# Performance work log

Measured on AMD Instinct MI355X. Metric: run time of the kernel, lower is better.

Reference implementation:

```python
import jax, jax.numpy as jnp
import numpy as np

N_NODES = 100000

def prelu(x, alpha):
    return jnp.where(x >= 0, x, alpha * x)

def setup_inputs() -> dict:
    key = jax.random.key(0)
    ks = jax.random.split(key, 8)
    N, E, D = N_NODES, 1600000, 128
    AX = jax.random.normal(ks[0], (N, D), dtype=jnp.float32)
    A_row = jax.random.randint(ks[1], (E,), 0, N, dtype=jnp.int32)
    A_col = jax.random.randint(ks[2], (E,), 0, N, dtype=jnp.int32)
    A_val = jax.random.uniform(ks[3], (E,), dtype=jnp.float32)
    # Xavier-uniform linear weights, zero bias (as in module init)
    lim = float(np.sqrt(6.0 / (D + D)))
    Wr_w = jax.random.uniform(ks[4], (D, D), minval=-lim, maxval=lim, dtype=jnp.float32)
    W_w = jax.random.uniform(ks[5], (D, D), minval=-lim, maxval=lim, dtype=jnp.float32)
    Wr_b = jnp.zeros((D,), dtype=jnp.float32)
    W_b = jnp.zeros((D,), dtype=jnp.float32)
    g_alpha = jnp.full((1,), 0.25, dtype=jnp.float32)    # PReLU default init
    act_alpha = jnp.full((1,), 0.25, dtype=jnp.float32)
    return {"AX": AX, "A_row": A_row, "A_col": A_col, "A_val": A_val,
            "Wr_w": Wr_w, "Wr_b": Wr_b, "W_w": W_w, "W_b": W_b,
            "g_alpha": g_alpha, "act_alpha": act_alpha}

def reference(AX, A_row, A_col, A_val, Wr_w, Wr_b, W_w, W_b, g_alpha, act_alpha):
    # h = g(Wr @ AX)  : [N, H]
    h = prelu(AX @ Wr_w.T + Wr_b, g_alpha)
    # SpMM: temp[i] = sum_{(i,j) in E} A_val * h[j]
    msgs = A_val[:, None] * h[A_col]                       # [E, H] gather
    temp = jax.ops.segment_sum(msgs, A_row, num_segments=N_NODES)
    # act(W @ temp), unsqueeze batch dim
    out = prelu(temp @ W_w.T + W_b, act_alpha)
    return out[None, :, :]
```

## Files before the change

kernel.cpp:

```cpp
#include <hip/hip_runtime.h>
#include <stdint.h>


typedef _Float16 half8 __attribute__((ext_vector_type(8)));
typedef _Float16 half4 __attribute__((ext_vector_type(4)));
typedef _Float16 half2v __attribute__((ext_vector_type(2)));
typedef float floatx4 __attribute__((ext_vector_type(4)));

#define LDK 136
#define SHIFT 5
#define NBMAX 3200
#define NBLK 256
#define SCT 1024
#define CAP 1024

__global__ __launch_bounds__(256, 2)
void gemm_hist(const float* __restrict__ X, const float* __restrict__ Wr,
               const float* __restrict__ bias, const float* __restrict__ alpha_p,
               _Float16* __restrict__ out, int N,
               const int* __restrict__ rows, int* __restrict__ hist_g,
               int E, int chunk, int NB,
               const float* __restrict__ W, _Float16* __restrict__ W16)
{
    __shared__ _Float16 Xs[128 * LDK];
    __shared__ _Float16 Ws[128 * LDK];
    const int tid = threadIdx.x;

    if (blockIdx.x < NBLK) {
        const int hb = blockIdx.x;
        int* lh = (int*)Xs;
        if (hb == 0) {
#pragma unroll
            for (int j = 0; j < 64; ++j)
                W16[tid + j * 256] = (_Float16)W[tid + j * 256];
        }
        for (int i = tid; i < NB; i += 256) lh[i] = 0;
        __syncthreads();
        int s = hb * chunk, e = min(E, s + chunk);
        for (int i = s + tid; i < e; i += 256)
            atomicAdd(&lh[rows[i] >> SHIFT], 1);
        __syncthreads();
        for (int b = tid; b < NB; b += 256)
            hist_g[b * NBLK + hb] = lh[b];
        return;
    }

    const int bm  = (blockIdx.x - NBLK) * 128;
    const float alpha = *alpha_p;

#pragma unroll
    for (int i = 0; i < 16; ++i) {
        int c   = tid + i * 256;
        int row = c >> 5;
        int coff = (c & 31) * 4;
        float4 f = *(const float4*)(Wr + row * 128 + coff);
        half4 hv = { (_Float16)f.x, (_Float16)f.y, (_Float16)f.z, (_Float16)f.w };
        *(half4*)(&Ws[row * LDK + coff]) = hv;
    }
#pragma unroll
    for (int i = 0; i < 16; ++i) {
        int c   = tid + i * 256;
        int row = c >> 5;
        int coff = (c & 31) * 4;
        int grow = bm + row;
        half4 hv = {};
        if (grow < N) {
            float4 f = *(const float4*)(X + (size_t)grow * 128 + coff);
            hv[0] = (_Float16)f.x; hv[1] = (_Float16)f.y;
            hv[2] = (_Float16)f.z; hv[3] = (_Float16)f.w;
        }
        *(half4*)(&Xs[row * LDK + coff]) = hv;
    }
    __syncthreads();

    const int wave = tid >> 6;
    const int lane = tid & 63;
    const int l15  = lane & 15;
    const int quad = lane >> 4;

    floatx4 acc[2][8] = {};
#pragma unroll
    for (int k0 = 0; k0 < 128; k0 += 32) {
        half8 a0 = *(const half8*)(&Xs[(wave * 32 +      l15) * LDK + k0 + quad * 8]);
        half8 a1 = *(const half8*)(&Xs[(wave * 32 + 16 + l15) * LDK + k0 + quad * 8]);
        half8 b[8];
#pragma unroll
        for (int n = 0; n < 8; ++n)
            b[n] = *(const half8*)(&Ws[(n * 16 + l15) * LDK + k0 + quad * 8]);
#pragma unroll
        for (int n = 0; n < 8; ++n) {
            acc[0][n] = __builtin_amdgcn_mfma_f32_16x16x32_f16(a0, b[n], acc[0][n], 0, 0, 0);
            acc[1][n] = __builtin_amdgcn_mfma_f32_16x16x32_f16(a1, b[n], acc[1][n], 0, 0, 0);
        }
    }

#pragma unroll
    for (int mt = 0; mt < 2; ++mt) {
#pragma unroll
        for (int n = 0; n < 8; ++n) {
#pragma unroll
            for (int r = 0; r < 4; ++r) {
                int row = bm + wave * 32 + mt * 16 + quad * 4 + r;
                int col = n * 16 + l15;
                if (row < N) {
                    float v = acc[mt][n][r] + bias[col];
                    v = (v >= 0.f) ? v : alpha * v;
                    out[(size_t)row * 128 + col] = (_Float16)v;
                }
            }
        }
    }
}

__global__ __launch_bounds__(NBLK)
void bucket_scan1(int* __restrict__ hist_g, int* __restrict__ tot)
{
    __shared__ int sd[NBLK];
    int b = blockIdx.x, t = threadIdx.x;
    int v = hist_g[b * NBLK + t];
    sd[t] = v;
    __syncthreads();
    for (int off = 1; off < NBLK; off <<= 1) {
        int x = (t >= off) ? sd[t - off] : 0;
        __syncthreads();
        sd[t] += x;
        __syncthreads();
    }
    hist_g[b * NBLK + t] = sd[t] - v;
    if (t == NBLK - 1) tot[b] = sd[t];
}

__global__ __launch_bounds__(1024)
void bucket_scan2(const int* __restrict__ tot, int* __restrict__ bkt_ptr, int NB, int E)
{
    __shared__ int sd[1024];
    int t = threadIdx.x;
    int v[4]; int s = 0;
#pragma unroll
    for (int j = 0; j < 4; ++j) {
        int idx = t * 4 + j;
        v[j] = (idx < NB) ? tot[idx] : 0;
        s += v[j];
    }
    sd[t] = s;
    __syncthreads();
    for (int off = 1; off < 1024; off <<= 1) {
        int x = (t >= off) ? sd[t - off] : 0;
        __syncthreads();
        sd[t] += x;
        __syncthreads();
    }
    int base = (t == 0) ? 0 : sd[t - 1];
#pragma unroll
    for (int j = 0; j < 4; ++j) {
        int idx = t * 4 + j;
        if (idx < NB) { bkt_ptr[idx] = base; base += v[j]; }
    }
    if (t == 0) bkt_ptr[NB] = E;
}

__global__ __launch_bounds__(SCT)
void bucket_scatter(const int* __restrict__ rows, const int* __restrict__ cols,
                    const float* __restrict__ vals, const int* __restrict__ bkt_ptr,
                    const int* __restrict__ hist_g, uint2* __restrict__ edges,
                    int E, int chunk, int NB)
{
    __shared__ int cur[NBMAX];
    int tid = threadIdx.x, blk = blockIdx.x;
    for (int b = tid; b < NB; b += SCT)
        cur[b] = bkt_ptr[b] + hist_g[b * NBLK + blk];
    __syncthreads();
    int s = blk * chunk, e = min(E, s + chunk);
    for (int i = s + tid; i < e; i += SCT) {
        int r = rows[i];
        int b = r >> SHIFT;
        uint2 ed;
        ed.x = (unsigned)cols[i] | ((unsigned)(r & 31) << 20);
        ed.y = __float_as_uint(vals[i]);
        int p = atomicAdd(&cur[b], 1);
        edges[p] = ed;
    }
}

__global__ __launch_bounds__(256, 8)
void spmm_fused(const int* __restrict__ bkt_ptr, const uint2* __restrict__ edges,
                const _Float16* __restrict__ h, const _Float16* __restrict__ W16,
                const float* __restrict__ bias, const float* __restrict__ alpha_p,
                float* __restrict__ out, int N)
{
    __shared__ uint2 eS[CAP];
    __shared__ _Float16 T[32 * LDK];
    __shared__ int bins[32], startS[33];

    const int tid  = threadIdx.x;
    const int wave = tid >> 6;
    const int lane = tid & 63;
    const int b    = blockIdx.x;
    const int s0   = bkt_ptr[b], e0 = bkt_ptr[b + 1];

    float acc[8][2] = {};

    for (int base = s0; base < e0; base += CAP) {
        const int n = min(CAP, e0 - base);
        if (tid < 32) bins[tid] = 0;
        __syncthreads();
        uint2 q[4];
#pragma unroll
        for (int u = 0; u < 4; ++u) {
            int i = tid + u * 256;
            if (i < n) {
                q[u] = edges[base + i];
                atomicAdd(&bins[q[u].x >> 20], 1);
            }
        }
        __syncthreads();
        if (tid < 32) {
            int x = bins[tid];
#pragma unroll
            for (int off = 1; off < 32; off <<= 1) {
                int y = __shfl_up(x, off);
                if (tid >= off) x += y;
            }
            startS[tid + 1] = x;
            if (tid == 0) startS[0] = 0;
            bins[tid] = x - bins[tid];
        }
        __syncthreads();
#pragma unroll
        for (int u = 0; u < 4; ++u) {
            int i = tid + u * 256;
            if (i < n) {
                int p = atomicAdd(&bins[q[u].x >> 20], 1);
                eS[p] = q[u];
            }
        }
        __syncthreads();

#pragma unroll
        for (int j = 0; j < 8; ++j) {
            int r  = wave * 8 + j;
            int rs = startS[r], re = startS[r + 1];
            float a0r = acc[j][0], a1r = acc[j][1];
            int i = rs;
            for (; i + 7 < re; i += 8) {
                uint2 q0 = eS[i],     q1 = eS[i + 1], q2 = eS[i + 2], q3 = eS[i + 3];
                uint2 q4 = eS[i + 4], q5 = eS[i + 5], q6 = eS[i + 6], q7 = eS[i + 7];
                half2v v0 = *(const half2v*)(h + (size_t)(q0.x & 0xFFFFF) * 128 + lane * 2);
                half2v v1 = *(const half2v*)(h + (size_t)(q1.x & 0xFFFFF) * 128 + lane * 2);
                half2v v2 = *(const half2v*)(h + (size_t)(q2.x & 0xFFFFF) * 128 + lane * 2);
                half2v v3 = *(const half2v*)(h + (size_t)(q3.x & 0xFFFFF) * 128 + lane * 2);
                half2v v4 = *(const half2v*)(h + (size_t)(q4.x & 0xFFFFF) * 128 + lane * 2);
                half2v v5 = *(const half2v*)(h + (size_t)(q5.x & 0xFFFFF) * 128 + lane * 2);
                half2v v6 = *(const half2v*)(h + (size_t)(q6.x & 0xFFFFF) * 128 + lane * 2);
                half2v v7 = *(const half2v*)(h + (size_t)(q7.x & 0xFFFFF) * 128 + lane * 2);
                float w0 = __uint_as_float(q0.y), w1 = __uint_as_float(q1.y);
                float w2 = __uint_as_float(q2.y), w3 = __uint_as_float(q3.y);
                float w4 = __uint_as_float(q4.y), w5 = __uint_as_float(q5.y);
                float w6 = __uint_as_float(q6.y), w7 = __uint_as_float(q7.y);
                a0r += w0 * (float)v0[0]; a1r += w0 * (float)v0[1];
                a0r += w1 * (float)v1[0]; a1r += w1 * (float)v1[1];
                a0r += w2 * (float)v2[0]; a1r += w2 * (float)v2[1];
                a0r += w3 * (float)v3[0]; a1r += w3 * (float)v3[1];
                a0r += w4 * (float)v4[0]; a1r += w4 * (float)v4[1];
                a0r += w5 * (float)v5[0]; a1r += w5 * (float)v5[1];
                a0r += w6 * (float)v6[0]; a1r += w6 * (float)v6[1];
                a0r += w7 * (float)v7[0]; a1r += w7 * (float)v7[1];
            }
            for (; i + 1 < re; i += 2) {
                uint2 q0 = eS[i], q1 = eS[i + 1];
                half2v v0 = *(const half2v*)(h + (size_t)(q0.x & 0xFFFFF) * 128 + lane * 2);
                half2v v1 = *(const half2v*)(h + (size_t)(q1.x & 0xFFFFF) * 128 + lane * 2);
                float w0 = __uint_as_float(q0.y), w1 = __uint_as_float(q1.y);
                a0r += w0 * (float)v0[0]; a1r += w0 * (float)v0[1];
                a0r += w1 * (float)v1[0]; a1r += w1 * (float)v1[1];
            }
            if (i < re) {
                uint2 q0 = eS[i];
                half2v v0 = *(const half2v*)(h + (size_t)(q0.x & 0xFFFFF) * 128 + lane * 2);
                float w0 = __uint_as_float(q0.y);
                a0r += w0 * (float)v0[0]; a1r += w0 * (float)v0[1];
            }
            acc[j][0] = a0r; acc[j][1] = a1r;
        }
        __syncthreads();
    }

#pragma unroll
    for (int j = 0; j < 8; ++j) {
        half2v o = { (_Float16)acc[j][0], (_Float16)acc[j][1] };
        *(half2v*)(&T[(wave * 8 + j) * LDK + lane * 2]) = o;
    }
    __syncthreads();

    const float alpha = *alpha_p;
    const int l15  = lane & 15;
    const int quad = lane >> 4;
    floatx4 c[2][2] = {};
#pragma unroll
    for (int k0 = 0; k0 < 128; k0 += 32) {
        half8 a0 = *(const half8*)(&T[(     l15) * LDK + k0 + quad * 8]);
        half8 a1 = *(const half8*)(&T[(16 + l15) * LDK + k0 + quad * 8]);
#pragma unroll
        for (int nt = 0; nt < 2; ++nt) {
            int nrow = (wave * 2 + nt) * 16 + l15;
            half8 bf = *(const half8*)(W16 + nrow * 128 + k0 + quad * 8);
            c[0][nt] = __builtin_amdgcn_mfma_f32_16x16x32_f16(a0, bf, c[0][nt], 0, 0, 0);
            c[1][nt] = __builtin_amdgcn_mfma_f32_16x16x32_f16(a1, bf, c[1][nt], 0, 0, 0);
        }
    }
    const int row0 = b << SHIFT;
#pragma unroll
    for (int mt = 0; mt < 2; ++mt) {
#pragma unroll
        for (int nt = 0; nt < 2; ++nt) {
            int col = (wave * 2 + nt) * 16 + l15;
            float bcol = bias[col];
#pragma unroll
            for (int r = 0; r < 4; ++r) {
                int row = row0 + mt * 16 + quad * 4 + r;
                if (row < N) {
                    float v = c[mt][nt][r] + bcol;
                    v = (v >= 0.f) ? v : alpha * v;
                    out[(size_t)row * 128 + col] = v;
                }
            }
        }
    }
}

static inline size_t align256(size_t x) { return (x + 255) & ~(size_t)255; }

extern "C" void kernel_launch(void* const* d_in, const int* in_sizes, int n_in,
                              void* d_out, int out_size, void* d_ws, size_t ws_size,
                              hipStream_t stream)
{
    const float* AX        = (const float*)d_in[0];
    const int*   A_row     = (const int*)  d_in[1];
    const int*   A_col     = (const int*)  d_in[2];
    const float* A_val     = (const float*)d_in[3];
    const float* Wr_w      = (const float*)d_in[4];
    const float* Wr_b      = (const float*)d_in[5];
    const float* W_w       = (const float*)d_in[6];
    const float* W_b       = (const float*)d_in[7];
    const float* g_alpha   = (const float*)d_in[8];
    const float* act_alpha = (const float*)d_in[9];

    const int N = in_sizes[0] / 128;
    const int E = in_sizes[1];
    const int NB = (N + 31) >> SHIFT;
    const int chunk = (E + NBLK - 1) / NBLK;

    char* ws = (char*)d_ws;
    size_t off = 0;
    _Float16* h       = (_Float16*)(ws + off); off += align256((size_t)N * 128 * 2);
    uint2*    edges   = (uint2*)   (ws + off); off += align256((size_t)E * 8);
    int*      hist_g  = (int*)     (ws + off); off += align256((size_t)NB * NBLK * 4);
    int*      tot     = (int*)     (ws + off); off += align256((size_t)NB * 4);
    int*      bkt_ptr = (int*)     (ws + off); off += align256((size_t)(NB + 1) * 4);
    _Float16* W16     = (_Float16*)(ws + off); off += align256((size_t)128 * 128 * 2);
    (void)ws_size; (void)n_in; (void)out_size;

    const int gemmB = (N + 127) / 128;

    gemm_hist<<<NBLK + gemmB, 256, 0, stream>>>(AX, Wr_w, Wr_b, g_alpha, h, N,
                                                A_row, hist_g, E, chunk, NB,
                                                W_w, W16);
    bucket_scan1<<<NB, NBLK, 0, stream>>>(hist_g, tot);
    bucket_scan2<<<1, 1024, 0, stream>>>(tot, bkt_ptr, NB, E);
    bucket_scatter<<<NBLK, SCT, 0, stream>>>(A_row, A_col, A_val, bkt_ptr, hist_g,
                                             edges, E, chunk, NB);
    spmm_fused<<<NB, 256, 0, stream>>>(bkt_ptr, edges, h, W16, W_b, act_alpha,
                                       (float*)d_out, N);
}
```

Before: 287.2 us.

## Load GEMM A-operand directly to registers and fold bucket scan2 into scatter

The GEMM blocks now load and convert X rows straight into MFMA A-fragment registers instead of staging them through shared memory. This halves the LDS footprint, so launch bounds go up to 3 blocks per SM. Separately, the single-block global bucket prefix scan is merged into bucket_scatter: each scatter block recomputes the 1024-wide scan redundantly, and block 0 writes bkt_ptr. This removes one kernel launch and a serialized tiny kernel, at the cost of redundant scan work in every scatter block and uncoalesced direct global loads for X.

```diff
diff --git a/kernel.cpp b/kernel.cpp
--- a/kernel.cpp
+++ b/kernel.cpp
@@ -14,7 +14,7 @@
 #define SCT 1024
 #define CAP 1024
 
-__global__ __launch_bounds__(256, 2)
+__global__ __launch_bounds__(256, 3)
 void gemm_hist(const float* __restrict__ X, const float* __restrict__ Wr,
                const float* __restrict__ bias, const float* __restrict__ alpha_p,
                _Float16* __restrict__ out, int N,
@@ -22,13 +22,12 @@
                int E, int chunk, int NB,
                const float* __restrict__ W, _Float16* __restrict__ W16)
 {
-    __shared__ _Float16 Xs[128 * LDK];
     __shared__ _Float16 Ws[128 * LDK];
     const int tid = threadIdx.x;
 
     if (blockIdx.x < NBLK) {
         const int hb = blockIdx.x;
-        int* lh = (int*)Xs;
+        int* lh = (int*)Ws;
         if (hb == 0) {
 #pragma unroll
             for (int j = 0; j < 64; ++j)
@@ -47,6 +46,31 @@
 
     const int bm  = (blockIdx.x - NBLK) * 128;
     const float alpha = *alpha_p;
+    const int wave = tid >> 6;
+    const int lane = tid & 63;
+    const int l15  = lane & 15;
+    const int quad = lane >> 4;
+
+    half8 a[2][4];
+#pragma unroll
+    for (int mt = 0; mt < 2; ++mt) {
+        const int xrow = bm + wave * 32 + mt * 16 + l15;
+        const float* xp = X + (size_t)xrow * 128 + quad * 8;
+        const bool ok = xrow < N;
+#pragma unroll
+        for (int k = 0; k < 4; ++k) {
+            half8 hv = {};
+            if (ok) {
+                float4 f0 = *(const float4*)(xp + k * 32);
+                float4 f1 = *(const float4*)(xp + k * 32 + 4);
+                hv[0] = (_Float16)f0.x; hv[1] = (_Float16)f0.y;
+                hv[2] = (_Float16)f0.z; hv[3] = (_Float16)f0.w;
+                hv[4] = (_Float16)f1.x; hv[5] = (_Float16)f1.y;
+                hv[6] = (_Float16)f1.z; hv[7] = (_Float16)f1.w;
+            }
+            a[mt][k] = hv;
+        }
+    }
 
 #pragma unroll
     for (int i = 0; i < 16; ++i) {
@@ -57,40 +81,20 @@
         half4 hv = { (_Float16)f.x, (_Float16)f.y, (_Float16)f.z, (_Float16)f.w };
         *(half4*)(&Ws[row * LDK + coff]) = hv;
     }
-#pragma unroll
-    for (int i = 0; i < 16; ++i) {
-        int c   = tid + i * 256;
-        int row = c >> 5;
-        int coff = (c & 31) * 4;
-        int grow = bm + row;
-        half4 hv = {};
-        if (grow < N) {
-            float4 f = *(const float4*)(X + (size_t)grow * 128 + coff);
-            hv[0] = (_Float16)f.x; hv[1] = (_Float16)f.y;
-            hv[2] = (_Float16)f.z; hv[3] = (_Float16)f.w;
-        }
-        *(half4*)(&Xs[row * LDK + coff]) = hv;
-    }
-    __syncthreads();
-
-    const int wave = tid >> 6;
-    const int lane = tid & 63;
-    const int l15  = lane & 15;
-    const int quad = lane >> 4;
+    __syncthreads();
 
     floatx4 acc[2][8] = {};
 #pragma unroll
-    for (int k0 = 0; k0 < 128; k0 += 32) {
-        half8 a0 = *(const half8*)(&Xs[(wave * 32 +      l15) * LDK + k0 + quad * 8]);
-        half8 a1 = *(const half8*)(&Xs[(wave * 32 + 16 + l15) * LDK + k0 + quad * 8]);
+    for (int k = 0; k < 4; ++k) {
+        const int k0 = k * 32;
         half8 b[8];
 #pragma unroll
         for (int n = 0; n < 8; ++n)
             b[n] = *(const half8*)(&Ws[(n * 16 + l15) * LDK + k0 + quad * 8]);
 #pragma unroll
         for (int n = 0; n < 8; ++n) {
-            acc[0][n] = __builtin_amdgcn_mfma_f32_16x16x32_f16(a0, b[n], acc[0][n], 0, 0, 0);
-            acc[1][n] = __builtin_amdgcn_mfma_f32_16x16x32_f16(a1, b[n], acc[1][n], 0, 0, 0);
+            acc[0][n] = __builtin_amdgcn_mfma_f32_16x16x32_f16(a[0][k], b[n], acc[0][n], 0, 0, 0);
+            acc[1][n] = __builtin_amdgcn_mfma_f32_16x16x32_f16(a[1][k], b[n], acc[1][n], 0, 0, 0);
         }
     }
 
@@ -130,11 +134,16 @@
     if (t == NBLK - 1) tot[b] = sd[t];
 }
 
-__global__ __launch_bounds__(1024)
-void bucket_scan2(const int* __restrict__ tot, int* __restrict__ bkt_ptr, int NB, int E)
-{
-    __shared__ int sd[1024];
-    int t = threadIdx.x;
+__global__ __launch_bounds__(SCT)
+void bucket_scatter(const int* __restrict__ rows, const int* __restrict__ cols,
+                    const float* __restrict__ vals, const int* __restrict__ tot,
+                    const int* __restrict__ hist_g, uint2* __restrict__ edges,
+                    int* __restrict__ bkt_ptr, int E, int chunk, int NB)
+{
+    __shared__ int sd[SCT];
+    __shared__ int cur[NBMAX];
+    const int t = threadIdx.x, blk = blockIdx.x;
+
     int v[4]; int s = 0;
 #pragma unroll
     for (int j = 0; j < 4; ++j) {
@@ -144,7 +153,7 @@
     }
     sd[t] = s;
     __syncthreads();
-    for (int off = 1; off < 1024; off <<= 1) {
+    for (int off = 1; off < SCT; off <<= 1) {
         int x = (t >= off) ? sd[t - off] : 0;
         __syncthreads();
         sd[t] += x;
@@ -154,24 +163,17 @@
 #pragma unroll
     for (int j = 0; j < 4; ++j) {
         int idx = t * 4 + j;
-        if (idx < NB) { bkt_ptr[idx] = base; base += v[j]; }
-    }
-    if (t == 0) bkt_ptr[NB] = E;
-}
-
-__global__ __launch_bounds__(SCT)
-void bucket_scatter(const int* __restrict__ rows, const int* __restrict__ cols,
-                    const float* __restrict__ vals, const int* __restrict__ bkt_ptr,
-                    const int* __restrict__ hist_g, uint2* __restrict__ edges,
-                    int E, int chunk, int NB)
-{
-    __shared__ int cur[NBMAX];
-    int tid = threadIdx.x, blk = blockIdx.x;
-    for (int b = tid; b < NB; b += SCT)
-        cur[b] = bkt_ptr[b] + hist_g[b * NBLK + blk];
-    __syncthreads();
-    int s = blk * chunk, e = min(E, s + chunk);
-    for (int i = s + tid; i < e; i += SCT) {
+        if (idx < NB) {
+            cur[idx] = base + hist_g[idx * NBLK + blk];
+            if (blk == 0) bkt_ptr[idx] = base;
+            base += v[j];
+        }
+    }
+    if (blk == 0 && t == 0) bkt_ptr[NB] = E;
+    __syncthreads();
+
+    int s0 = blk * chunk, e0 = min(E, s0 + chunk);
+    for (int i = s0 + t; i < e0; i += SCT) {
         int r = rows[i];
         int b = r >> SHIFT;
         uint2 ed;
@@ -366,9 +368,8 @@
                                                 A_row, hist_g, E, chunk, NB,
                                                 W_w, W16);
     bucket_scan1<<<NB, NBLK, 0, stream>>>(hist_g, tot);
-    bucket_scan2<<<1, 1024, 0, stream>>>(tot, bkt_ptr, NB, E);
-    bucket_scatter<<<NBLK, SCT, 0, stream>>>(A_row, A_col, A_val, bkt_ptr, hist_g,
-                                             edges, E, chunk, NB);
+    bucket_scatter<<<NBLK, SCT, 0, stream>>>(A_row, A_col, A_val, tot, hist_g,
+                                             edges, bkt_ptr, E, chunk, NB);
     spmm_fused<<<NB, 256, 0, stream>>>(bkt_ptr, edges, h, W16, W_b, act_alpha,
                                        (float*)d_out, N);
 }
```

Result: faster. 266.7 us (-7.1%).
